# Kernel tuning notes

Measured on AMD Instinct MI355X. Metric: run time of the kernel, lower is better.

The kernel has to match this reference:

```python
import jax, jax.numpy as jnp
import numpy as np
from math import comb

K = 10            # Bernstein polynomial order
N = 100000        # num nodes
E = 3200000       # num edges


def _bern_prop(x, row, col, temp):
    """BernNet propagation: sum_k relu(temp)_k * C(K,k)/2^K * L^k (2I-L)^{K-k} x,
    with L = I - D^{-1/2} A D^{-1/2} built from the directed edge list."""
    theta = jax.nn.relu(temp)
    deg = jax.ops.segment_sum(jnp.ones((row.shape[0],), dtype=x.dtype), row, num_segments=N)
    dinv = jnp.where(deg > 0, jax.lax.rsqrt(deg), jnp.zeros_like(deg))
    w = (dinv[row] * dinv[col])[:, None]  # normalized adjacency edge weights [E,1]

    def adj(v):  # A_hat @ v : gather-multiply-scatter over edges
        return jax.ops.segment_sum(v[col] * w, row, num_segments=N)

    # tmp[i] = (2I - L)^i x = (I + A_hat)^i x
    tmp = [x]
    v = x
    for _ in range(K):
        v = v + adj(v)
        tmp.append(v)

    scale = 1.0 / (2 ** K)
    out = (comb(K, 0) * scale) * theta[0] * tmp[K]
    for i in range(K):
        v = tmp[K - i - 1]
        for _ in range(i + 1):  # apply L = I - A_hat, (i+1) times
            v = v - adj(v)
        out = out + (comb(K, i + 1) * scale) * theta[i + 1] * v
    return out


def setup_inputs() -> dict:
    key = jax.random.key(0)
    ks = jax.random.split(key, 5)
    x = jax.random.normal(ks[0], (N, 512), dtype=jnp.float32)
    edge_index = jax.random.randint(ks[1], (2, E), 0, N, dtype=jnp.int32)
    W1 = jax.random.normal(ks[2], (512, 256), dtype=jnp.float32) * 0.04
    b1 = jnp.zeros((256,), jnp.float32)
    W2 = jax.random.normal(ks[3], (256, 64), dtype=jnp.float32) * 0.06
    b2 = jnp.zeros((64,), jnp.float32)
    temp = jnp.ones((K + 1,), jnp.float32)  # Bern_prop param, initialized to ones
    return {"x": x, "edge_index": edge_index, "W1": W1, "b1": b1, "W2": W2, "b2": b2, "temp": temp}


def reference(x, edge_index, W1, b1, W2, b2, temp):
    # eval mode: dropout is identity; self.m (BatchNorm) is never called in forward
    row, col = edge_index[0], edge_index[1]
    h = jax.nn.relu(x @ W1 + b1)   # lin1 + relu
    h = h @ W2 + b2                # lin2 -> [N, num_classes]
    h = _bern_prop(h, row, col, temp)
    return jax.nn.log_softmax(h, axis=1)
```

## Files before the change

### kernel.cpp

```cpp
#include <hip/hip_runtime.h>
#include <hip/hip_bf16.h>
#include <hip/hip_cooperative_groups.h>

namespace cg = cooperative_groups;

#define K_ORDER 10
#define NNODES  100000
#define NEDGES  3200000

typedef __bf16 bf16x8 __attribute__((ext_vector_type(8)));
typedef float  floatx4 __attribute__((ext_vector_type(4)));
typedef short  short8v __attribute__((ext_vector_type(8)));

struct WS {
  float* d;
  int*   jmax;
  int*   cnt;
  int*   off;
  int*   cursor;
  float* dinv;
  int*   csr_col;
  float* csr_w;
  float* h2;
  float* buf0;
  float* buf1;
  short* w1s;
  short* w2s;
  int*   bsum;
  int*   bbase;
};

__device__ inline short f2bf(float f) {
  __hip_bfloat16 h = __float2bfloat16(f);
  return __builtin_bit_cast(short, h);
}

__device__ inline bf16x8 pack8(const float4& lo, const float4& hi) {
  short8v t;
  t[0] = f2bf(lo.x); t[1] = f2bf(lo.y); t[2] = f2bf(lo.z); t[3] = f2bf(lo.w);
  t[4] = f2bf(hi.x); t[5] = f2bf(hi.y); t[6] = f2bf(hi.z); t[7] = f2bf(hi.w);
  return __builtin_bit_cast(bf16x8, t);
}

__device__ inline void swz_body(const float* __restrict__ W, short* __restrict__ dst,
                                int Kd, int Nd, int t) {
  int lane = t & 63, frag = t >> 6;
  int nfr = Nd >> 4;
  int kt = frag / nfr, nc = frag - kt * nfr;
  int m16 = lane & 15, q = lane >> 4;
  int kbase = kt * 32 + q * 8;
  int col = nc * 16 + m16;
  short v[8];
#pragma unroll
  for (int j = 0; j < 8; ++j) v[j] = f2bf(W[(size_t)(kbase + j) * Nd + col]);
  short4* o = (short4*)&dst[(size_t)t * 8];
  o[0] = make_short4(v[0], v[1], v[2], v[3]);
  o[1] = make_short4(v[4], v[5], v[6], v[7]);
}

__global__ __launch_bounds__(256) void k_swzall(const float* __restrict__ W1,
    const float* __restrict__ W2, const float* __restrict__ temp, WS ws) {
  int b = blockIdx.x;
  if (b < 64) {
    swz_body(W1, ws.w1s, 512, 256, b * 256 + threadIdx.x);
  } else if (b < 72) {
    swz_body(W2, ws.w2s, 256, 64, (b - 64) * 256 + threadIdx.x);
  } else if (threadIdx.x == 0) {
    const double C10[11] = {1,10,45,120,210,252,210,120,45,10,1};
    double dd[11];
    for (int j = 0; j <= K_ORDER; ++j) dd[j] = 0.0;
    for (int k = 0; k <= K_ORDER; ++k) {
      double th = temp[k] > 0.f ? (double)temp[k] : 0.0;
      double c  = th * C10[k] / 1024.0;
      double p[11];
      for (int j = 0; j <= K_ORDER; ++j) p[j] = 0.0;
      p[0] = 1.0;
      int deg = 0;
      for (int i = 0; i < K_ORDER - k; ++i) {
        ++deg;
        for (int j = deg; j >= 1; --j) p[j] += p[j-1];
      }
      for (int i = 0; i < k; ++i) {
        ++deg;
        for (int j = deg; j >= 1; --j) p[j] = p[j] - p[j-1];
      }
      for (int j = 0; j <= K_ORDER; ++j) dd[j] += c * p[j];
    }
    int jm = 0;
    for (int j = 1; j <= K_ORDER; ++j) if (dd[j] != 0.0) jm = j;
    for (int j = 0; j <= K_ORDER; ++j) ws.d[j] = (float)dd[j];
    *ws.jmax = jm;
  }
}

__global__ __launch_bounds__(256) void k_fwd(const float* __restrict__ A,
    const float* __restrict__ b1, const float* __restrict__ b2,
    WS ws, float* __restrict__ out)
{
  __shared__ short H1s[64 * 264];
  const int tid = threadIdx.x;
  const int wave = tid >> 6, lane = tid & 63;
  const int q = lane >> 4, m16 = lane & 15;
  const int bm = blockIdx.x * 64;

  const float* arow[4];
#pragma unroll
  for (int r = 0; r < 4; ++r) {
    int grow = bm + r * 16 + m16; if (grow > NNODES - 1) grow = NNODES - 1;
    arow[r] = A + (size_t)grow * 512 + q * 8;
  }
  const short* bcol = ws.w1s + ((size_t)(wave * 4) * 64 + lane) * 8;

  floatx4 acc[4][4] = {};

  float4 pa[4][2];
  bf16x8 pb[4];
#pragma unroll
  for (int r = 0; r < 4; ++r) {
    pa[r][0] = *(const float4*)(arow[r]);
    pa[r][1] = *(const float4*)(arow[r] + 4);
  }
#pragma unroll
  for (int c = 0; c < 4; ++c) pb[c] = *(const bf16x8*)(bcol + c * 512);

#pragma unroll 1
  for (int kt = 0; kt < 16; ++kt) {
    bf16x8 af[4], bf[4];
#pragma unroll
    for (int r = 0; r < 4; ++r) af[r] = pack8(pa[r][0], pa[r][1]);
#pragma unroll
    for (int c = 0; c < 4; ++c) bf[c] = pb[c];
    if (kt < 15) {
#pragma unroll
      for (int r = 0; r < 4; ++r) {
        pa[r][0] = *(const float4*)(arow[r] + (kt + 1) * 32);
        pa[r][1] = *(const float4*)(arow[r] + (kt + 1) * 32 + 4);
      }
      const short* bn = bcol + (size_t)(kt + 1) * 8192;
#pragma unroll
      for (int c = 0; c < 4; ++c) pb[c] = *(const bf16x8*)(bn + c * 512);
    }
#pragma unroll
    for (int r = 0; r < 4; ++r)
#pragma unroll
      for (int c = 0; c < 4; ++c)
        acc[r][c] = __builtin_amdgcn_mfma_f32_16x16x32_bf16(af[r], bf[c], acc[r][c], 0, 0, 0);
  }

  float bv[4];
#pragma unroll
  for (int c = 0; c < 4; ++c) bv[c] = b1[wave * 64 + c * 16 + m16];
#pragma unroll
  for (int r = 0; r < 4; ++r)
#pragma unroll
    for (int c = 0; c < 4; ++c)
#pragma unroll
      for (int reg = 0; reg < 4; ++reg)
        H1s[(r * 16 + q * 4 + reg) * 264 + wave * 64 + c * 16 + m16] =
            f2bf(fmaxf(acc[r][c][reg] + bv[c], 0.f));
  __syncthreads();

  floatx4 acc2[4] = {};
#pragma unroll
  for (int kt = 0; kt < 8; ++kt) {
    bf16x8 af2 = *(const bf16x8*)&H1s[(wave * 16 + m16) * 264 + kt * 32 + q * 8];
    const short* bb = ws.w2s + ((size_t)(kt * 4) * 64 + lane) * 8;
#pragma unroll
    for (int c = 0; c < 4; ++c) {
      bf16x8 bf2 = *(const bf16x8*)(bb + c * 512);
      acc2[c] = __builtin_amdgcn_mfma_f32_16x16x32_bf16(af2, bf2, acc2[c], 0, 0, 0);
    }
  }

  int jm = *ws.jmax;
  float d0 = ws.d[0];
  float bv2[4];
#pragma unroll
  for (int c = 0; c < 4; ++c) bv2[c] = b2[c * 16 + m16];

  if (jm > 0) {
#pragma unroll
    for (int reg = 0; reg < 4; ++reg) {
      int rowm = bm + wave * 16 + q * 4 + reg;
      if (rowm < NNODES) {
        size_t o = (size_t)rowm * 64 + m16;
#pragma unroll
        for (int c = 0; c < 4; ++c)
          ws.h2[o + c * 16] = acc2[c][reg] + bv2[c];
      }
    }
  } else {
#pragma unroll
    for (int reg = 0; reg < 4; ++reg) {
      float v[4];
#pragma unroll
      for (int c = 0; c < 4; ++c) v[c] = d0 * (acc2[c][reg] + bv2[c]);
      float m = fmaxf(fmaxf(v[0], v[1]), fmaxf(v[2], v[3]));
#pragma unroll
      for (int o = 1; o < 16; o <<= 1) m = fmaxf(m, __shfl_xor(m, o));
      float s = 0.f;
#pragma unroll
      for (int c = 0; c < 4; ++c) s += __expf(v[c] - m);
#pragma unroll
      for (int o = 1; o < 16; o <<= 1) s += __shfl_xor(s, o);
      float ls = __logf(s);
      int rowm = bm + wave * 16 + q * 4 + reg;
      if (rowm < NNODES) {
        size_t o = (size_t)rowm * 64 + m16;
#pragma unroll
        for (int c = 0; c < 4; ++c) out[o + c * 16] = v[c] - m - ls;
      }
    }
  }
}

__global__ __launch_bounds__(256) void k_graph(const int* __restrict__ ei,
                                               WS ws, float* __restrict__ out) {
  const int jm = *ws.jmax;
  if (jm == 0) return;
  cg::grid_group g = cg::this_grid();
  const int t = threadIdx.x;
  const int gtid = blockIdx.x * 256 + t;
  const int gstride = 512 * 256;

  for (int i = gtid; i < NNODES; i += gstride) { ws.cnt[i] = 0; ws.cursor[i] = 0; }
  {
    float s = ws.d[jm];
    float* dst = (jm & 1) ? ws.buf1 : ws.buf0;
    for (int i = gtid; i < NNODES * 64; i += gstride) dst[i] = s * ws.h2[i];
  }
  g.sync();

  for (int e = gtid; e < NEDGES; e += gstride) atomicAdd(&ws.cnt[ei[e]], 1);
  g.sync();

  __shared__ int sd[256];
  const int i3 = blockIdx.x * 256 + t;
  {
    int v = (i3 < NNODES) ? ws.cnt[i3] : 0;
    if (i3 < NNODES) ws.dinv[i3] = v > 0 ? rsqrtf((float)v) : 0.f;
    sd[t] = v;
    __syncthreads();
    for (int o = 1; o < 256; o <<= 1) {
      int a = (t >= o) ? sd[t - o] : 0;
      __syncthreads();
      sd[t] += a;
      __syncthreads();
    }
    if (i3 < NNODES) ws.off[i3 + 1] = sd[t];
    if (t == 255) ws.bsum[blockIdx.x] = sd[255];
    if (blockIdx.x == 0 && t == 0) ws.off[0] = 0;
  }
  g.sync();

  if (blockIdx.x == 0) {
    __shared__ int sd2[512];
    sd2[t] = ws.bsum[t]; sd2[t + 256] = ws.bsum[t + 256];
    __syncthreads();
    if (t == 0) {
      int run = 0;
      for (int b = 0; b < 512; ++b) { int x = sd2[b]; sd2[b] = run; run += x; }
    }
    __syncthreads();
    ws.bbase[t] = sd2[t]; ws.bbase[t + 256] = sd2[t + 256];
  }
  g.sync();

  if (i3 < NNODES) ws.off[i3 + 1] += ws.bbase[blockIdx.x];
  g.sync();

  for (int e = gtid; e < NEDGES; e += gstride) {
    int row = ei[e], col = ei[NEDGES + e];
    float wv = ws.dinv[row] * ws.dinv[col];
    int pos = ws.off[row] + atomicAdd(&ws.cursor[row], 1);
    ws.csr_col[pos] = col;
    ws.csr_w[pos]   = wv;
  }
  g.sync();

  const int lane = t & 63;
  const int wid0 = blockIdx.x * 4 + (t >> 6);
  const int nwaves = 512 * 4;
  for (int j = jm - 1; j >= 0; --j) {
    const float* src = ((j + 1) & 1) ? ws.buf1 : ws.buf0;
    float*       dst = (j & 1)       ? ws.buf1 : ws.buf0;
    float dj = ws.d[j];
    for (int node = wid0; node < NNODES; node += nwaves) {
      int s = ws.off[node], e = ws.off[node + 1];
      float acc = 0.f;
      for (int base = s; base < e; base += 64) {
        int idx = base + lane;
        int cc = 0; float cw = 0.f;
        if (idx < e) { cc = ws.csr_col[idx]; cw = ws.csr_w[idx]; }
        int n = min(64, e - base);
        for (int u = 0; u < n; ++u) {
          int   c2 = __shfl(cc, u);
          float w2 = __shfl(cw, u);
          acc += w2 * src[(size_t)c2 * 64 + lane];
        }
      }
      dst[(size_t)node * 64 + lane] = acc + dj * ws.h2[(size_t)node * 64 + lane];
    }
    g.sync();
  }

  for (int node = wid0; node < NNODES; node += nwaves) {
    size_t idx = (size_t)node * 64 + lane;
    float v = ws.buf0[idx];
    float m = v;
#pragma unroll
    for (int o = 32; o > 0; o >>= 1) m = fmaxf(m, __shfl_xor(m, o));
    float s = __expf(v - m);
#pragma unroll
    for (int o = 32; o > 0; o >>= 1) s += __shfl_xor(s, o);
    out[idx] = (v - m) - __logf(s);
  }
}

extern "C" void kernel_launch(void* const* d_in, const int* in_sizes, int n_in,
                              void* d_out, int out_size, void* d_ws, size_t ws_size,
                              hipStream_t stream) {
  const float* x    = (const float*)d_in[0];
  const int*   ei   = (const int*)  d_in[1];
  const float* W1   = (const float*)d_in[2];
  const float* b1   = (const float*)d_in[3];
  const float* W2   = (const float*)d_in[4];
  const float* b2   = (const float*)d_in[5];
  const float* temp = (const float*)d_in[6];
  float* out = (float*)d_out;

  char* w = (char*)d_ws;
  size_t o = 0;
  auto bump = [&](size_t bytes) { size_t r = o; o += (bytes + 255) & ~(size_t)255; return r; };
  WS ws;
  ws.d       = (float*)(w + bump(11 * 4));
  ws.jmax    = (int*)  (w + bump(4));
  ws.cnt     = (int*)  (w + bump((size_t)NNODES * 4));
  ws.off     = (int*)  (w + bump((size_t)(NNODES + 1) * 4));
  ws.cursor  = (int*)  (w + bump((size_t)NNODES * 4));
  ws.dinv    = (float*)(w + bump((size_t)NNODES * 4));
  ws.csr_col = (int*)  (w + bump((size_t)NEDGES * 4));
  ws.csr_w   = (float*)(w + bump((size_t)NEDGES * 4));
  ws.h2      = (float*)(w + bump((size_t)NNODES * 64 * 4));
  ws.buf0    = (float*)(w + bump((size_t)NNODES * 64 * 4));
  ws.buf1    = (float*)(w + bump((size_t)NNODES * 64 * 4));
  ws.w1s     = (short*)(w + bump((size_t)512 * 256 * 2));
  ws.w2s     = (short*)(w + bump((size_t)256 * 64 * 2));
  ws.bsum    = (int*)  (w + bump(512 * 4));
  ws.bbase   = (int*)  (w + bump(512 * 4));

  const int MBLK = (NNODES + 63) / 64;

  k_swzall<<<73, 256, 0, stream>>>(W1, W2, temp, ws);
  k_fwd<<<MBLK, 256, 0, stream>>>(x, b1, b2, ws, out);

  void* args[] = { (void*)&ei, (void*)&ws, (void*)&out };
  hipLaunchCooperativeKernel((void*)k_graph, dim3(512), dim3(256), args, 0, stream);
}
```

Before: 429.7 us.

## Stage x tiles into LDS via async global_load_lds with triple buffering

```diff
diff --git a/kernel.cpp b/kernel.cpp
--- a/kernel.cpp
+++ b/kernel.cpp
@@ -97,59 +97,90 @@
     const float* __restrict__ b1, const float* __restrict__ b2,
     WS ws, float* __restrict__ out)
 {
-  __shared__ short H1s[64 * 264];
+  __shared__ __align__(16) char smem[64 * 264 * 2];
+  short* H1s = (short*)smem;
   const int tid = threadIdx.x;
   const int wave = tid >> 6, lane = tid & 63;
   const int q = lane >> 4, m16 = lane & 15;
   const int bm = blockIdx.x * 64;
 
-  const float* arow[4];
-#pragma unroll
-  for (int r = 0; r < 4; ++r) {
-    int grow = bm + r * 16 + m16; if (grow > NNODES - 1) grow = NNODES - 1;
-    arow[r] = A + (size_t)grow * 512 + q * 8;
-  }
+  const int s0 = wave * 128 + lane, s1 = s0 + 64;
+  const int row0 = s0 >> 3, row1 = s1 >> 3;
+  const int kgs0 = (s0 & 7) ^ (row0 & 7);
+  const int kgs1 = (s1 & 7) ^ (row1 & 7);
+  int gr0 = bm + row0; if (gr0 > NNODES - 1) gr0 = NNODES - 1;
+  int gr1 = bm + row1; if (gr1 > NNODES - 1) gr1 = NNODES - 1;
+  const float* gp0 = A + (size_t)gr0 * 512 + kgs0 * 4;
+  const float* gp1 = A + (size_t)gr1 * 512 + kgs1 * 4;
+  __attribute__((address_space(3))) char* lbase =
+      (__attribute__((address_space(3))) char*)smem;
+  const unsigned lo0 = (unsigned)(wave * 2) * 1024u;
+  const unsigned lo1 = lo0 + 1024u;
+
+  const int rx = m16 & 7;
+  const unsigned cs0 = (unsigned)((2 * q) ^ rx) * 16u;
+  const unsigned cs1 = (unsigned)((2 * q + 1) ^ rx) * 16u;
+
   const short* bcol = ws.w1s + ((size_t)(wave * 4) * 64 + lane) * 8;
 
+#define STAGE(KT, BUF) do { \
+    __builtin_amdgcn_global_load_lds( \
+      (const __attribute__((address_space(1))) void*)(gp0 + (KT) * 32), \
+      (__attribute__((address_space(3))) void*)(lbase + (BUF) * 8192 + lo0), 16, 0, 0); \
+    __builtin_amdgcn_global_load_lds( \
+      (const __attribute__((address_space(1))) void*)(gp1 + (KT) * 32), \
+      (__attribute__((address_space(3))) void*)(lbase + (BUF) * 8192 + lo1), 16, 0, 0); \
+  } while (0)
+
   floatx4 acc[4][4] = {};
 
-  float4 pa[4][2];
+  STAGE(0, 0);
+  STAGE(1, 1);
+  asm volatile("" ::: "memory");
   bf16x8 pb[4];
-#pragma unroll
-  for (int r = 0; r < 4; ++r) {
-    pa[r][0] = *(const float4*)(arow[r]);
-    pa[r][1] = *(const float4*)(arow[r] + 4);
-  }
 #pragma unroll
   for (int c = 0; c < 4; ++c) pb[c] = *(const bf16x8*)(bcol + c * 512);
 
 #pragma unroll 1
   for (int kt = 0; kt < 16; ++kt) {
-    bf16x8 af[4], bf[4];
-#pragma unroll
-    for (int r = 0; r < 4; ++r) af[r] = pack8(pa[r][0], pa[r][1]);
-#pragma unroll
-    for (int c = 0; c < 4; ++c) bf[c] = pb[c];
+    if (kt < 15) asm volatile("s_waitcnt vmcnt(6)" ::: "memory");
+    else         asm volatile("s_waitcnt vmcnt(4)" ::: "memory");
+    __builtin_amdgcn_s_barrier();
+    asm volatile("" ::: "memory");
+
+    if (kt < 14) STAGE(kt + 2, (kt + 2) % 3);
+    bf16x8 pbn[4];
     if (kt < 15) {
-#pragma unroll
-      for (int r = 0; r < 4; ++r) {
-        pa[r][0] = *(const float4*)(arow[r] + (kt + 1) * 32);
-        pa[r][1] = *(const float4*)(arow[r] + (kt + 1) * 32 + 4);
-      }
       const short* bn = bcol + (size_t)(kt + 1) * 8192;
 #pragma unroll
-      for (int c = 0; c < 4; ++c) pb[c] = *(const bf16x8*)(bn + c * 512);
+      for (int c = 0; c < 4; ++c) pbn[c] = *(const bf16x8*)(bn + c * 512);
+    }
+
+    const char* bufp = (const char*)smem + (kt % 3) * 8192;
+    bf16x8 af[4];
+#pragma unroll
+    for (int r = 0; r < 4; ++r) {
+      const char* rp = bufp + (unsigned)(r * 16 + m16) * 128u;
+      float4 vlo = *(const float4*)(rp + cs0);
+      float4 vhi = *(const float4*)(rp + cs1);
+      af[r] = pack8(vlo, vhi);
     }
 #pragma unroll
     for (int r = 0; r < 4; ++r)
 #pragma unroll
       for (int c = 0; c < 4; ++c)
-        acc[r][c] = __builtin_amdgcn_mfma_f32_16x16x32_bf16(af[r], bf[c], acc[r][c], 0, 0, 0);
-  }
+        acc[r][c] = __builtin_amdgcn_mfma_f32_16x16x32_bf16(af[r], pb[c], acc[r][c], 0, 0, 0);
+    if (kt < 15) {
+#pragma unroll
+      for (int c = 0; c < 4; ++c) pb[c] = pbn[c];
+    }
+  }
+#undef STAGE
 
   float bv[4];
 #pragma unroll
   for (int c = 0; c < 4; ++c) bv[c] = b1[wave * 64 + c * 16 + m16];
+  __syncthreads();
 #pragma unroll
   for (int r = 0; r < 4; ++r)
 #pragma unroll
```

Result: faster. 407.3 us (-5.2%).
